# Kernel optimization log

Hardware: AMD Instinct MI355X
Metric: run time of the kernel (lower is better)

The kernel has to match this reference:

```python
import jax, jax.numpy as jnp
import numpy as np

H = 1024      # hidden_dim
NH = 16       # num_heads
HD = H // NH  # head_dim
FF = 4096     # ff_dim
EPS = 1e-6


def layer_norm(x, gamma, beta):
    # faithful to source: unbiased std (ddof=1), divide by (std + eps)
    mean = jnp.mean(x, axis=-1, keepdims=True)
    var = jnp.sum((x - mean) ** 2, axis=-1, keepdims=True) / (x.shape[-1] - 1)
    std = jnp.sqrt(var)
    return gamma * (x - mean) / (std + EPS) + beta


def linear_mulbias(x, W, b):
    # source LinearLayer: einsum('...i,io,o->...o') -> (x @ W) * b (bias MULTIPLIES)
    return jnp.einsum('bti,io->bto', x, W) * b


def setup_inputs() -> dict:
    key = jax.random.key(0)
    ks = jax.random.split(key, 11)
    B, T = 2, 2048
    return {
        'x':      jax.random.normal(ks[0], (B, T, H), jnp.float32),
        'Wqkv':   jax.random.normal(ks[1], (H, 3 * H), jnp.float32),
        'bqkv':   jax.random.normal(ks[2], (3 * H,), jnp.float32),
        'W1':     jax.random.normal(ks[3], (H, FF), jnp.float32),
        'b1':     jax.random.normal(ks[4], (FF,), jnp.float32),
        'W2':     jax.random.normal(ks[5], (FF, H), jnp.float32),
        'b2':     jax.random.normal(ks[6], (H,), jnp.float32),
        'gamma1': jax.random.normal(ks[7], (H,), jnp.float32),
        'beta1':  jax.random.normal(ks[8], (H,), jnp.float32),
        'gamma2': jax.random.normal(ks[9], (H,), jnp.float32),
        'beta2':  jax.random.normal(ks[10], (H,), jnp.float32),
    }


def attention(x, Wqkv, bqkv):
    B, T, _ = x.shape
    qkv = linear_mulbias(x, Wqkv, bqkv)                 # [B,T,3H]
    # einops 'b t (d k h) -> k b h t d' with k=3, h=NH: last dim decomposes (d,3,h)
    qkv = qkv.reshape(B, T, HD, 3, NH)
    qkv = jnp.transpose(qkv, (3, 0, 4, 1, 2))           # [3,B,NH,T,HD]
    q, k, v = qkv[0], qkv[1], qkv[2]
    scores = jnp.einsum('bhid,bhjd->bhij', q, k) / (H ** 0.5)  # scale by full hidden_dim
    attn = jax.nn.softmax(scores, axis=-1)
    out = jnp.einsum('bhij,bhjd->bhid', attn, v)        # [B,NH,T,HD]
    return jnp.transpose(out, (0, 2, 1, 3)).reshape(B, T, H)


def reference(x, Wqkv, bqkv, W1, b1, W2, b2, gamma1, beta1, gamma2, beta2):
    # dropout is identity in eval mode
    out = layer_norm(x + attention(x, Wqkv, bqkv), gamma1, beta1)
    ffn = linear_mulbias(jnp.maximum(linear_mulbias(out, W1, b1), 0.0), W2, b2)
    out = layer_norm(out + ffn, gamma2, beta2)
    return out
```

## Files before the change

### kernel.cpp

```cpp
#include <hip/hip_runtime.h>
#include <math.h>

#define B 2
#define T 2048
#define H 1024
#define NH 16
#define HD 64
#define FF 4096
#define M_TOK (B*T)
#define LOG2E 1.4426950408889634f

typedef unsigned short u16;
typedef __attribute__((ext_vector_type(8))) short bf16x8;
typedef __attribute__((ext_vector_type(4))) float f32x4;

#define WAITBAR3  asm volatile("s_waitcnt vmcnt(3)\n\ts_barrier" ::: "memory")
#define WAITBAR4  asm volatile("s_waitcnt vmcnt(4)\n\ts_barrier" ::: "memory")
#define WAITBAR0  asm volatile("s_waitcnt vmcnt(0)\n\ts_barrier" ::: "memory")

__device__ __forceinline__ u16 f2bf(float f) {
  union { float f; unsigned u; } v; v.f = f;
  const unsigned r = (v.u + 0x7FFFu + ((v.u >> 16) & 1u)) >> 16;
  return (u16)r;
}
__device__ __forceinline__ float bf2f(u16 h) {
  union { unsigned u; float f; } v; v.u = ((unsigned)h) << 16;
  return v.f;
}
__device__ __forceinline__ unsigned cvt_pk_bf16(float lo, float hi) {
  unsigned r;
  asm("v_cvt_pk_bf16_f32 %0, %1, %2" : "=v"(r) : "v"(lo), "v"(hi));
  return r;
}
__device__ __forceinline__ float m3(float a, float b, float c) {
  return fmaxf(fmaxf(a, b), c);
}
__device__ __forceinline__ void gload16(const u16* g, u16* l) {
  __builtin_amdgcn_global_load_lds(
      (const __attribute__((address_space(1))) unsigned int*)g,
      (__attribute__((address_space(3))) unsigned int*)l, 16, 0, 0);
}

__global__ __launch_bounds__(256) void preprocess(
    const float* __restrict__ x, u16* __restrict__ xh, u16* __restrict__ xl,
    const float* __restrict__ Wqkv, u16* __restrict__ WqTh, u16* __restrict__ WqTl,
    const float* __restrict__ W1_, u16* __restrict__ W1T_,
    const float* __restrict__ W2_, u16* __restrict__ W2T_)
{
  const int bid = blockIdx.x;
  const int tid = threadIdx.x;
  if (bid < 4096) {
    const size_t i = ((size_t)bid * 256 + tid) * 4;
    const float4 v = *(const float4*)(x + i);
    union { u16 s[4]; uint2 u; } h, l;
    const float f[4] = {v.x, v.y, v.z, v.w};
#pragma unroll
    for (int j = 0; j < 4; ++j) {
      const u16 hb = f2bf(f[j]); h.s[j] = hb; l.s[j] = f2bf(f[j] - bf2f(hb));
    }
    *(uint2*)(xh + i) = h.u;
    *(uint2*)(xl + i) = l.u;
    return;
  }
  __shared__ float tile[64][69];
  const float* in; u16* oh; u16* ol = nullptr; int K, N, k0, n0, split = 0;
  if (bid < 4864) {
    const int tb = bid - 4096;
    in = Wqkv; oh = WqTh; ol = WqTl; K = H; N = 3*H; split = 1;
    n0 = (tb % 48) * 64; k0 = (tb / 48) * 64;
  } else if (bid < 5888) {
    const int tb = bid - 4864;
    in = W1_; oh = W1T_; K = H; N = FF;
    n0 = (tb & 63) * 64; k0 = (tb >> 6) * 64;
  } else {
    const int tb = bid - 5888;
    in = W2_; oh = W2T_; K = FF; N = H;
    n0 = (tb & 15) * 64; k0 = (tb >> 4) * 64;
  }
  const int r = tid >> 4, c4 = (tid & 15) * 4;
#pragma unroll
  for (int i = 0; i < 4; ++i) {
    const float4 v = *(const float4*)(in + (size_t)(k0 + i*16 + r) * N + n0 + c4);
    tile[i*16+r][c4]   = v.x; tile[i*16+r][c4+1] = v.y;
    tile[i*16+r][c4+2] = v.z; tile[i*16+r][c4+3] = v.w;
  }
  __syncthreads();
  const int n = tid >> 2, kq = tid & 3;
  union { u16 s[8]; int4 v; } ph0, ph1, pl0, pl1;
#pragma unroll
  for (int j = 0; j < 8; ++j) {
    const float f0 = tile[kq*16 + j][n];
    const float f1 = tile[kq*16 + 8 + j][n];
    const u16 h0 = f2bf(f0), h1 = f2bf(f1);
    ph0.s[j] = h0; ph1.s[j] = h1;
    if (split) { pl0.s[j] = f2bf(f0 - bf2f(h0)); pl1.s[j] = f2bf(f1 - bf2f(h1)); }
  }
  u16* po = oh + (size_t)(n0 + n) * K + k0 + kq * 16;
  *(int4*)po = ph0.v; *(int4*)(po + 8) = ph1.v;
  if (split) {
    u16* pl = ol + (size_t)(n0 + n) * K + k0 + kq * 16;
    *(int4*)pl = pl0.v; *(int4*)(pl + 8) = pl1.v;
  }
}

__device__ __forceinline__ int swz(int r, int kq) {
  return r * 32 + ((kq ^ ((r >> 1) & 3)) * 8);
}

template<int SPLIT, int RELU, int OBF, int QKV3, int DEEP3, int PARTIAL>
__global__ __launch_bounds__(256) void mfma_gemm(
    const u16* __restrict__ Ah, const u16* __restrict__ Al,
    const u16* __restrict__ Bh, const u16* __restrict__ Bl,
    const float* __restrict__ bias,
    float* __restrict__ Cf, u16* __restrict__ Cb,
    int M, int N, int K)
{
  __shared__ u16 lds[DEEP3 ? 24576 : (SPLIT ? 32768 : 16384)];
  const int BUFSZ = SPLIT ? 16384 : 8192;
  const int tid = threadIdx.x;
  const int bid = blockIdx.x;
  const int xcd = bid & 7;
  const int idx = bid >> 3;
  const int row0 = (xcd * 4 + (idx & 3)) * 128;
  const int col0 = (idx >> 2) * 128;
  const int wv = tid >> 6, lane = tid & 63;
  const int wr = wv >> 1, wc = wv & 1;
  const int kq = lane >> 4, fr = lane & 15;

  int kb = 0, kE = K;
  if (PARTIAL) {
    const int khf = blockIdx.y;
    kb = khf * (K >> 1); kE = kb + (K >> 1);
    Cf += (size_t)khf * ((size_t)M * N);
  }

  f32x4 acc[4][4] = {};

#define GSTAGE(lbase, gb, rowbase, kk) do { \
    _Pragma("unroll") \
    for (int t_ = 0; t_ < 2; ++t_) { \
      const int c_ = wv * 2 + t_; \
      const int idx_ = c_ * 64 + lane; \
      const int r_ = idx_ >> 2; \
      const int kq_ = (idx_ & 3) ^ ((r_ >> 1) & 3); \
      gload16((gb) + (size_t)((rowbase) + r_) * K + (kk) + kq_ * 8, \
              &lds[(lbase) + c_ * 512]); \
    } } while (0)

#define BLSTAGE(lbase, kk) do { \
    _Pragma("unroll") \
    for (int t_ = 0; t_ < 2; ++t_) { \
      const int c_ = wv * 2 + t_; \
      if (!QKV3 || ((((col0 >> 4) + c_) % 3) != 2)) { \
        const int idx_ = c_ * 64 + lane; \
        const int r_ = idx_ >> 2; \
        const int kq_ = (idx_ & 3) ^ ((r_ >> 1) & 3); \
        gload16(Bl + (size_t)(col0 + r_) * K + (kk) + kq_ * 8, \
                &lds[(lbase) + c_ * 512]); \
      } } } while (0)

  if (DEEP3) {
    const int nk = (kE - kb) >> 5;
    GSTAGE(0, Ah, row0, kb);            GSTAGE(4096, Bh, col0, kb);
    GSTAGE(8192, Ah, row0, kb + 32);    GSTAGE(8192 + 4096, Bh, col0, kb + 32);
    WAITBAR4;
    int cslot = 0, islot = 2;
    for (int i = 0; i < nk; ++i) {
      if (i + 2 < nk) {
        const int kk = kb + (i + 2) * 32;
        GSTAGE(islot * 8192, Ah, row0, kk);
        GSTAGE(islot * 8192 + 4096, Bh, col0, kk);
        islot = (islot == 2) ? 0 : islot + 1;
      }
      const int rb = cslot * 8192;
      bf16x8 a_h[4];
#pragma unroll
      for (int m = 0; m < 4; ++m)
        a_h[m] = *(const bf16x8*)&lds[rb + swz(wr*64 + m*16 + fr, kq)];
#pragma unroll
      for (int n = 0; n < 4; ++n) {
        const bf16x8 b_h = *(const bf16x8*)&lds[rb + 4096 + swz(wc*64 + n*16 + fr, kq)];
#pragma unroll
        for (int m = 0; m < 4; ++m)
          acc[m][n] = __builtin_amdgcn_mfma_f32_16x16x32_bf16(a_h[m], b_h, acc[m][n], 0, 0, 0);
      }
      cslot = (cslot == 2) ? 0 : cslot + 1;
      if (i + 1 < nk) { if (i + 2 < nk) WAITBAR4; else WAITBAR0; }
    }
  } else {
    GSTAGE(0, Ah, row0, kb);
    GSTAGE(4096, Bh, col0, kb);
    if (SPLIT) { GSTAGE(8192, Al, row0, kb); BLSTAGE(12288, kb); }
    __syncthreads();

    int cur = 0;
    for (int k0 = kb; k0 < kE; k0 += 32) {
      const int nxt = cur ^ 1;
      if (k0 + 32 < kE) {
        GSTAGE(nxt*BUFSZ, Ah, row0, k0 + 32);
        GSTAGE(nxt*BUFSZ + 4096, Bh, col0, k0 + 32);
        if (SPLIT) { GSTAGE(nxt*BUFSZ + 8192, Al, row0, k0 + 32);
                     BLSTAGE(nxt*BUFSZ + 12288, k0 + 32); }
      }
      const int rb = cur * BUFSZ;
      bf16x8 a_h[4], a_l[4];
#pragma unroll
      for (int m = 0; m < 4; ++m) {
        a_h[m] = *(const bf16x8*)&lds[rb + swz(wr*64 + m*16 + fr, kq)];
        if (SPLIT) a_l[m] = *(const bf16x8*)&lds[rb + 8192 + swz(wr*64 + m*16 + fr, kq)];
      }
#pragma unroll
      for (int n = 0; n < 4; ++n) {
        const bf16x8 b_h = *(const bf16x8*)&lds[rb + 4096 + swz(wc*64 + n*16 + fr, kq)];
#pragma unroll
        for (int m = 0; m < 4; ++m)
          acc[m][n] = __builtin_amdgcn_mfma_f32_16x16x32_bf16(a_h[m], b_h, acc[m][n], 0, 0, 0);
        if (SPLIT) {
          const bool dolo = !QKV3 || ((((col0 >> 4) + wc * 4 + n) % 3) != 2);
          if (dolo) {
            const bf16x8 b_l = *(const bf16x8*)&lds[rb + 12288 + swz(wc*64 + n*16 + fr, kq)];
#pragma unroll
            for (int m = 0; m < 4; ++m) {
              acc[m][n] = __builtin_amdgcn_mfma_f32_16x16x32_bf16(a_h[m], b_l, acc[m][n], 0, 0, 0);
              acc[m][n] = __builtin_amdgcn_mfma_f32_16x16x32_bf16(a_l[m], b_h, acc[m][n], 0, 0, 0);
            }
          }
        }
      }
      __syncthreads();
      cur = nxt;
    }
  }
#undef GSTAGE
#undef BLSTAGE

  const int orow0 = row0 + wr * 64, ocol0 = col0 + wc * 64;
#pragma unroll
  for (int n = 0; n < 4; ++n) {
    const int col = ocol0 + n * 16 + fr;
    const float bs = PARTIAL ? 1.0f : bias[col];
#pragma unroll
    for (int m = 0; m < 4; ++m) {
      const int rbase = orow0 + m * 16 + (lane >> 4) * 4;
#pragma unroll
      for (int j = 0; j < 4; ++j) {
        float v = acc[m][n][j] * bs;
        if (RELU) v = fmaxf(v, 0.0f);
        const size_t off = (size_t)(rbase + j) * N + col;
        if (OBF) Cb[off] = f2bf(v); else Cf[off] = v;
      }
    }
  }
}

__global__ __launch_bounds__(256) void repack_qkv(
    const float* __restrict__ qkv,
    u16* __restrict__ Qh, u16* __restrict__ Ql,
    u16* __restrict__ Kh, u16* __restrict__ Kl, u16* __restrict__ Vb)
{
  const int bt = blockIdx.x;
  const int b = bt >> 11, t = bt & (T - 1);
  const int tid = threadIdx.x;
  __shared__ float Ls[3 * H];
  const float* src = qkv + (size_t)bt * (3 * H);
#pragma unroll
  for (int i = 0; i < 3; ++i) {
    const int c4 = i * 256 + tid;
    *(float4*)&Ls[c4 * 4] = *(const float4*)(src + c4 * 4);
  }
  __syncthreads();
  const float qscale = LOG2E / 32.0f;
#pragma unroll
  for (int i = 0; i < 4; ++i) {
    const int j = i * 256 + tid;
    const int h = j >> 6, d = j & 63;
    const size_t dst = (((size_t)(b * NH + h)) * T + t) * HD + d;
    const float q = Ls[d * 48 + h] * qscale;
    const u16 qhb = f2bf(q);
    Qh[dst] = qhb; Ql[dst] = f2bf(q - bf2f(qhb));
    const float k = Ls[d * 48 + 16 + h];
    const u16 khb = f2bf(k);
    Kh[dst] = khb; Kl[dst] = f2bf(k - bf2f(khb));
    Vb[dst] = f2bf(Ls[d * 48 + 32 + h]);
  }
}

__global__ __launch_bounds__(256) void vtrans(
    const u16* __restrict__ Vb, u16* __restrict__ VT)
{
  __shared__ u16 Ls[64][72];
  const int bh = blockIdx.y, t0 = blockIdx.x * 64;
  const int tid = threadIdx.x;
  const int r = tid >> 2, c = (tid & 3) * 16;
  const size_t src = ((size_t)bh * T + t0 + r) * HD + c;
  *(int4*)&Ls[r][c]     = *(const int4*)(Vb + src);
  *(int4*)&Ls[r][c + 8] = *(const int4*)(Vb + src + 8);
  __syncthreads();
  const int d = tid >> 2, tc = (tid & 3) * 16;
  u16 buf[16];
#pragma unroll
  for (int i = 0; i < 16; ++i) buf[i] = Ls[tc + i][d];
  u16* dst = VT + ((size_t)bh * HD + d) * T + t0 + tc;
  *(int4*)dst       = *(int4*)&buf[0];
  *(int4*)(dst + 8) = *(int4*)&buf[8];
}

__device__ __forceinline__ int sigma_k(int r) {
  return ((r >> 5) << 5) | (((r >> 2) & 3) << 3) | (((r >> 4) & 1) << 2) | (r & 3);
}

__global__ __launch_bounds__(512, 4) void flash_attn_mfma(
    const u16* __restrict__ Qh, const u16* __restrict__ Ql,
    const u16* __restrict__ Kh, const u16* __restrict__ Kl,
    const u16* __restrict__ VT, float* __restrict__ Out)
{
  __shared__ u16 sm[3 * 12288];
  const int i = blockIdx.x;
  const int slot = i >> 3;
  const int bh = (i & 7) * 4 + (slot >> 4);
  const int row0 = (slot & 15) * 128;
  const int b = bh >> 4, h = bh & 15;
  const int tid = threadIdx.x, wave = tid >> 6, lane = tid & 63;
  const int fr = lane & 15, kq = lane >> 4;

  bf16x8 qh[2], ql[2];
  const size_t qoff = ((size_t)bh * T + row0 + wave*16 + fr) * HD + kq*8;
#pragma unroll
  for (int ks = 0; ks < 2; ++ks) {
    qh[ks] = *(const bf16x8*)(Qh + qoff + ks*32);
    ql[ks] = *(const bf16x8*)(Ql + qoff + ks*32);
  }

  bf16x8 ones8;
#pragma unroll
  for (int z = 0; z < 8; ++z) ones8[z] = (short)0x3F80;

  f32x4 o[4] = {};
  f32x4 oex = {};
  float m_ = -1e30f;

  const int c_ = wave;
  const int r0_ = c_ * 8 + (lane >> 3), s_ = lane & 7;
  const int cd0 = s_ ^ (r0_ & 7);
  const int k0_ = sigma_k(r0_);
  const u16* pKh0 = Kh + ((size_t)bh*T + k0_)*HD + cd0*8;
  const u16* pKl0 = Kl + ((size_t)bh*T + k0_)*HD + cd0*8;
  const u16* pV0  = VT + ((size_t)bh*HD + r0_)*T + cd0*8;

#define FSTAGE(sb) do { \
    gload16(pKh0, &sm[(sb) + c_*512]); \
    gload16(pKl0, &sm[(sb) + 4096 + c_*512]); \
    gload16(pV0,  &sm[(sb) + 8192 + c_*512]); \
    pKh0 += 64*HD; pKl0 += 64*HD; pV0 += 64; \
  } while (0)

  FSTAGE(0);
  FSTAGE(12288);
  WAITBAR3;
  int cslot = 0, islot = 2;

  const int NT = T / 64;
  for (int t = 0; t < NT; ++t) {
    if (t + 2 < NT) {
      FSTAGE(islot * 12288);
      islot = (islot == 2) ? 0 : islot + 1;
    }
    const u16* smb = &sm[cslot * 12288];

    f32x4 s[4] = {};
    __builtin_amdgcn_s_setprio(1);
#pragma unroll
    for (int ks = 0; ks < 2; ++ks) {
#pragma unroll
      for (int n = 0; n < 4; ++n) {
        const int kr = n * 16 + fr;
        const int sl = ((ks*4 + kq) ^ (kr & 7)) * 8;
        const bf16x8 kh_ = *(const bf16x8*)&smb[kr*64 + sl];
        const bf16x8 kl_ = *(const bf16x8*)&smb[4096 + kr*64 + sl];
        s[n] = __builtin_amdgcn_mfma_f32_16x16x32_bf16(kh_, qh[ks], s[n], 0, 0, 0);
        s[n] = __builtin_amdgcn_mfma_f32_16x16x32_bf16(kl_, qh[ks], s[n], 0, 0, 0);
        s[n] = __builtin_amdgcn_mfma_f32_16x16x32_bf16(kh_, ql[ks], s[n], 0, 0, 0);
      }
    }
    __builtin_amdgcn_s_setprio(0);

    const float g0 = m3(s[0][0], s[0][1], s[0][2]);
    const float g1 = m3(s[0][3], s[1][0], s[1][1]);
    const float g2 = m3(s[1][2], s[1][3], s[2][0]);
    const float g3 = m3(s[2][1], s[2][2], s[2][3]);
    const float g4 = m3(s[3][0], s[3][1], s[3][2]);
    float mx = fmaxf(m3(g0, g1, g2), m3(g3, g4, s[3][3]));
    mx = fmaxf(mx, __shfl_xor(mx, 16));
    mx = fmaxf(mx, __shfl_xor(mx, 32));
    if (!__all(mx <= m_ + 8.0f)) {
      const float mn = fmaxf(m_, mx);
      const float fsc = exp2f(m_ - mn);
      m_ = mn;
#pragma unroll
      for (int n = 0; n < 4; ++n) {
        o[n][0] *= fsc; o[n][1] *= fsc;
        o[n][2] *= fsc; o[n][3] *= fsc;
      }
      oex[0] *= fsc; oex[1] *= fsc; oex[2] *= fsc; oex[3] *= fsc;
    }

    float p[4][4];
#pragma unroll
    for (int n = 0; n < 4; ++n)
#pragma unroll
      for (int jj = 0; jj < 4; ++jj)
        p[n][jj] = exp2f(s[n][jj] - m_);

    unsigned pk[4][2];
#pragma unroll
    for (int n = 0; n < 4; ++n) {
      pk[n][0] = cvt_pk_bf16(p[n][0], p[n][1]);
      pk[n][1] = cvt_pk_bf16(p[n][2], p[n][3]);
    }

    __builtin_amdgcn_s_setprio(1);
#pragma unroll
    for (int ks = 0; ks < 2; ++ks) {
      union { unsigned u[4]; bf16x8 v; } pb;
      pb.u[0] = pk[2*ks][0];   pb.u[1] = pk[2*ks][1];
      pb.u[2] = pk[2*ks+1][0]; pb.u[3] = pk[2*ks+1][1];
#pragma unroll
      for (int n = 0; n < 4; ++n) {
        const int dr = n * 16 + fr;
        const bf16x8 vf = *(const bf16x8*)&smb[8192 + dr*64 + (((ks*4 + kq) ^ (dr & 7)) * 8)];
        o[n] = __builtin_amdgcn_mfma_f32_16x16x32_bf16(vf, pb.v, o[n], 0, 0, 0);
      }
      oex = __builtin_amdgcn_mfma_f32_16x16x32_bf16(ones8, pb.v, oex, 0, 0, 0);
    }
    __builtin_amdgcn_s_setprio(0);

    cslot = (cslot == 2) ? 0 : cslot + 1;
    if (t + 1 < NT) { if (t + 2 < NT) WAITBAR3; else WAITBAR0; }
  }
#undef FSTAGE

  {
    const float inv = 1.0f / oex[0];
    const size_t qrow = (size_t)b * T + row0 + wave*16 + fr;
#pragma unroll
    for (int n = 0; n < 4; ++n) {
      float4 ov;
      ov.x = o[n][0] * inv; ov.y = o[n][1] * inv;
      ov.z = o[n][2] * inv; ov.w = o[n][3] * inv;
      *(float4*)(Out + qrow * H + h * HD + n * 16 + kq * 4) = ov;
    }
  }
}

__global__ __launch_bounds__(256) void ln_residual(
    const float* __restrict__ A, const float* __restrict__ Bz,
    const float* __restrict__ gamma, const float* __restrict__ beta,
    u16* __restrict__ obf)
{
  const int row = blockIdx.x, tid = threadIdx.x;
  const int wave = tid >> 6, lane = tid & 63;
  const size_t off = (size_t)row * H + tid * 4;
  const float4 av = *(const float4*)(A + off);
  const float4 bv = *(const float4*)(Bz + off);
  float4 y; y.x = av.x + bv.x; y.y = av.y + bv.y; y.z = av.z + bv.z; y.w = av.w + bv.w;
  float s  = y.x + y.y + y.z + y.w;
  float ss = y.x*y.x + y.y*y.y + y.z*y.z + y.w*y.w;
#pragma unroll
  for (int o = 32; o >= 1; o >>= 1) { s += __shfl_xor(s, o); ss += __shfl_xor(ss, o); }
  __shared__ float red[2][4];
  if (lane == 0) { red[0][wave] = s; red[1][wave] = ss; }
  __syncthreads();
  s  = red[0][0] + red[0][1] + red[0][2] + red[0][3];
  ss = red[1][0] + red[1][1] + red[1][2] + red[1][3];
  const float mean = s * (1.0f / (float)H);
  float var = (ss - (float)H * mean * mean) * (1.0f / (float)(H - 1));
  var = fmaxf(var, 0.0f);
  const float inv = 1.0f / (sqrtf(var) + 1e-6f);
  const float4 gv = *(const float4*)(gamma + tid * 4);
  const float4 be = *(const float4*)(beta + tid * 4);
  float4 o;
  o.x = gv.x * (y.x - mean) * inv + be.x;
  o.y = gv.y * (y.y - mean) * inv + be.y;
  o.z = gv.z * (y.z - mean) * inv + be.z;
  o.w = gv.w * (y.w - mean) * inv + be.w;
  union { u16 s[4]; uint2 u; } pk;
  pk.s[0] = f2bf(o.x); pk.s[1] = f2bf(o.y); pk.s[2] = f2bf(o.z); pk.s[3] = f2bf(o.w);
  *(uint2*)(obf + off) = pk.u;
}

__global__ __launch_bounds__(256) void ln_residual_sk(
    const u16* __restrict__ Ab, const float* __restrict__ PA,
    const float* __restrict__ PB, const float* __restrict__ bb,
    const float* __restrict__ gamma, const float* __restrict__ beta,
    float* __restrict__ out)
{
  const int row = blockIdx.x, tid = threadIdx.x;
  const int wave = tid >> 6, lane = tid & 63;
  const size_t off = (size_t)row * H + tid * 4;
  union { uint2 u; u16 s[4]; } au;
  au.u = *(const uint2*)(Ab + off);
  const float4 pa = *(const float4*)(PA + off);
  const float4 pb = *(const float4*)(PB + off);
  const float4 bw = *(const float4*)(bb + tid * 4);
  float4 y;
  y.x = bf2f(au.s[0]) + (pa.x + pb.x) * bw.x;
  y.y = bf2f(au.s[1]) + (pa.y + pb.y) * bw.y;
  y.z = bf2f(au.s[2]) + (pa.z + pb.z) * bw.z;
  y.w = bf2f(au.s[3]) + (pa.w + pb.w) * bw.w;
  float s  = y.x + y.y + y.z + y.w;
  float ss = y.x*y.x + y.y*y.y + y.z*y.z + y.w*y.w;
#pragma unroll
  for (int o = 32; o >= 1; o >>= 1) { s += __shfl_xor(s, o); ss += __shfl_xor(ss, o); }
  __shared__ float red[2][4];
  if (lane == 0) { red[0][wave] = s; red[1][wave] = ss; }
  __syncthreads();
  s  = red[0][0] + red[0][1] + red[0][2] + red[0][3];
  ss = red[1][0] + red[1][1] + red[1][2] + red[1][3];
  const float mean = s * (1.0f / (float)H);
  float var = (ss - (float)H * mean * mean) * (1.0f / (float)(H - 1));
  var = fmaxf(var, 0.0f);
  const float inv = 1.0f / (sqrtf(var) + 1e-6f);
  const float4 gv = *(const float4*)(gamma + tid * 4);
  const float4 be = *(const float4*)(beta + tid * 4);
  float4 o;
  o.x = gv.x * (y.x - mean) * inv + be.x;
  o.y = gv.y * (y.y - mean) * inv + be.y;
  o.z = gv.z * (y.z - mean) * inv + be.z;
  o.w = gv.w * (y.w - mean) * inv + be.w;
  *(float4*)(out + off) = o;
}

extern "C" void kernel_launch(void* const* d_in, const int* in_sizes, int n_in,
                              void* d_out, int out_size, void* d_ws, size_t ws_size,
                              hipStream_t stream)
{
  const float* x    = (const float*)d_in[0];
  const float* Wqkv = (const float*)d_in[1];
  const float* bqkv = (const float*)d_in[2];
  const float* W1   = (const float*)d_in[3];
  const float* b1   = (const float*)d_in[4];
  const float* W2   = (const float*)d_in[5];
  const float* b2   = (const float*)d_in[6];
  const float* g1   = (const float*)d_in[7];
  const float* be1  = (const float*)d_in[8];
  const float* g2   = (const float*)d_in[9];
  const float* be2  = (const float*)d_in[10];
  float* out = (float*)d_out;
  char* w = (char*)d_ws;

  float* qkv  = (float*)(w + 0);
  u16*   h1b  = (u16*)  (w + 0);
  u16*   xh   = (u16*)  (w + 52428800);
  u16*   xl   = (u16*)  (w + 60817408);
  u16*   Qh   = (u16*)  (w + 52428800);
  u16*   Ql   = (u16*)  (w + 60817408);
  u16*   WqTh = (u16*)  (w + 69206016);
  u16*   WqTl = (u16*)  (w + 75497472);
  u16*   Khb  = (u16*)  (w + 69206016);
  u16*   Klb  = (u16*)  (w + 77594624);
  u16*   Vbb  = (u16*)  (w + 85983232);
  u16*   VTb  = (u16*)  (w + 94371840);
  float* pAB  = (float*)(w + 52428800);
  float* attn = (float*)(w + 102760448);
  u16*   W1T  = (u16*)  (w + 119537664);
  u16*   W2T  = (u16*)  (w + 127926272);
  u16*   ln1b = (u16*)  (w + 136314880);

  preprocess<<<6912, 256, 0, stream>>>(x, xh, xl, Wqkv, WqTh, WqTl,
                                       W1, W1T, W2, W2T);
  mfma_gemm<1,0,0,1,0,0><<<24 * 32, 256, 0, stream>>>(xh, xl, WqTh, WqTl, bqkv,
                                                      qkv, nullptr, M_TOK, 3*H, H);
  repack_qkv<<<M_TOK, 256, 0, stream>>>(qkv, Qh, Ql, Khb, Klb, Vbb);
  vtrans<<<dim3(T/64, B*NH), 256, 0, stream>>>(Vbb, VTb);
  flash_attn_mfma<<<512, 512, 0, stream>>>(Qh, Ql, Khb, Klb, VTb, attn);
  ln_residual<<<M_TOK, 256, 0, stream>>>(x, attn, g1, be1, ln1b);
  mfma_gemm<0,1,1,0,1,0><<<32 * 32, 256, 0, stream>>>(ln1b, nullptr, W1T, nullptr, b1,
                                                      nullptr, h1b, M_TOK, FF, H);
  mfma_gemm<0,0,0,0,1,1><<<dim3(8 * 32, 2), 256, 0, stream>>>(h1b, nullptr, W2T, nullptr, nullptr,
                                                              pAB, nullptr, M_TOK, H, FF);
  ln_residual_sk<<<M_TOK, 256, 0, stream>>>(ln1b, pAB, pAB + 4194304, b2, g2, be2, out);
}
```

Baseline: 296.6 us.

## Fuse FFN2 split-K halves in-block via LDS and vectorize QKV repack

Replaces the two-block split-K FFN2 GEMM, which wrote two partial fp32 outputs, with a 512-thread kernel. Two wave groups each cover half of K and their accumulators are reduced through LDS, with bias and residual applied in the epilogue. The final LN then only reads one fp32 buffer instead of two partials plus the bf16 residual. Separately, repack_qkv pads its LDS row to avoid bank conflicts and writes 4-element packed stores instead of scalar u16 stores. The costs are larger LDS per block and fewer blocks in flight for FFN2 (256 blocks of 512 threads).

Measured after the change: 292.2 us. No clear change (-1.5%).

```diff
diff --git a/kernel.cpp b/kernel.cpp
--- a/kernel.cpp
+++ b/kernel.cpp
@@ -107,7 +107,7 @@
   return r * 32 + ((kq ^ ((r >> 1) & 3)) * 8);
 }
 
-template<int SPLIT, int RELU, int OBF, int QKV3, int DEEP3, int PARTIAL>
+template<int SPLIT, int RELU, int OBF, int QKV3, int DEEP3>
 __global__ __launch_bounds__(256) void mfma_gemm(
     const u16* __restrict__ Ah, const u16* __restrict__ Al,
     const u16* __restrict__ Bh, const u16* __restrict__ Bl,
@@ -127,13 +127,6 @@
   const int wr = wv >> 1, wc = wv & 1;
   const int kq = lane >> 4, fr = lane & 15;
 
-  int kb = 0, kE = K;
-  if (PARTIAL) {
-    const int khf = blockIdx.y;
-    kb = khf * (K >> 1); kE = kb + (K >> 1);
-    Cf += (size_t)khf * ((size_t)M * N);
-  }
-
   f32x4 acc[4][4] = {};
 
 #define GSTAGE(lbase, gb, rowbase, kk) do { \
@@ -160,14 +153,14 @@
       } } } while (0)
 
   if (DEEP3) {
-    const int nk = (kE - kb) >> 5;
-    GSTAGE(0, Ah, row0, kb);            GSTAGE(4096, Bh, col0, kb);
-    GSTAGE(8192, Ah, row0, kb + 32);    GSTAGE(8192 + 4096, Bh, col0, kb + 32);
+    const int nk = K >> 5;
+    GSTAGE(0, Ah, row0, 0);            GSTAGE(4096, Bh, col0, 0);
+    GSTAGE(8192, Ah, row0, 32);        GSTAGE(8192 + 4096, Bh, col0, 32);
     WAITBAR4;
     int cslot = 0, islot = 2;
     for (int i = 0; i < nk; ++i) {
       if (i + 2 < nk) {
-        const int kk = kb + (i + 2) * 32;
+        const int kk = (i + 2) * 32;
         GSTAGE(islot * 8192, Ah, row0, kk);
         GSTAGE(islot * 8192 + 4096, Bh, col0, kk);
         islot = (islot == 2) ? 0 : islot + 1;
@@ -188,15 +181,15 @@
       if (i + 1 < nk) { if (i + 2 < nk) WAITBAR4; else WAITBAR0; }
     }
   } else {
-    GSTAGE(0, Ah, row0, kb);
-    GSTAGE(4096, Bh, col0, kb);
-    if (SPLIT) { GSTAGE(8192, Al, row0, kb); BLSTAGE(12288, kb); }
+    GSTAGE(0, Ah, row0, 0);
+    GSTAGE(4096, Bh, col0, 0);
+    if (SPLIT) { GSTAGE(8192, Al, row0, 0); BLSTAGE(12288, 0); }
     __syncthreads();
 
     int cur = 0;
-    for (int k0 = kb; k0 < kE; k0 += 32) {
+    for (int k0 = 0; k0 < K; k0 += 32) {
       const int nxt = cur ^ 1;
-      if (k0 + 32 < kE) {
+      if (k0 + 32 < K) {
         GSTAGE(nxt*BUFSZ, Ah, row0, k0 + 32);
         GSTAGE(nxt*BUFSZ + 4096, Bh, col0, k0 + 32);
         if (SPLIT) { GSTAGE(nxt*BUFSZ + 8192, Al, row0, k0 + 32);
@@ -238,7 +231,7 @@
 #pragma unroll
   for (int n = 0; n < 4; ++n) {
     const int col = ocol0 + n * 16 + fr;
-    const float bs = PARTIAL ? 1.0f : bias[col];
+    const float bs = bias[col];
 #pragma unroll
     for (int m = 0; m < 4; ++m) {
       const int rbase = orow0 + m * 16 + (lane >> 4) * 4;
@@ -253,6 +246,101 @@
   }
 }
 
+__global__ __launch_bounds__(512, 2) void mfma_ffn2(
+    const u16* __restrict__ Ah, const u16* __restrict__ Bh,
+    const u16* __restrict__ Res, const float* __restrict__ bias,
+    float* __restrict__ Y)
+{
+  const int N = H, K = FF;
+  __shared__ u16 lds[2 * 24576];
+  const int tid = threadIdx.x;
+  const int bid = blockIdx.x;
+  const int xcd = bid & 7;
+  const int idx = bid >> 3;
+  const int row0 = (xcd * 4 + (idx & 3)) * 128;
+  const int col0 = (idx >> 2) * 128;
+  const int wv8 = tid >> 6, lane = tid & 63;
+  const int grp = wv8 >> 2, wv = wv8 & 3;
+  const int wr = wv >> 1, wc = wv & 1;
+  const int kq = lane >> 4, fr = lane & 15;
+  const int kb = grp * (K >> 1);
+  u16* gl = &lds[grp * 24576];
+
+  f32x4 acc[4][4] = {};
+
+#define GSTAGE2(lbase, gb, rowbase, kk) do { \
+    _Pragma("unroll") \
+    for (int t_ = 0; t_ < 2; ++t_) { \
+      const int c_ = wv * 2 + t_; \
+      const int idx_ = c_ * 64 + lane; \
+      const int r_ = idx_ >> 2; \
+      const int kq_ = (idx_ & 3) ^ ((r_ >> 1) & 3); \
+      gload16((gb) + (size_t)((rowbase) + r_) * K + (kk) + kq_ * 8, \
+              &gl[(lbase) + c_ * 512]); \
+    } } while (0)
+
+  const int nk = (K >> 1) >> 5;
+  GSTAGE2(0, Ah, row0, kb);            GSTAGE2(4096, Bh, col0, kb);
+  GSTAGE2(8192, Ah, row0, kb + 32);    GSTAGE2(8192 + 4096, Bh, col0, kb + 32);
+  WAITBAR4;
+  int cslot = 0, islot = 2;
+  for (int i = 0; i < nk; ++i) {
+    if (i + 2 < nk) {
+      const int kk = kb + (i + 2) * 32;
+      GSTAGE2(islot * 8192, Ah, row0, kk);
+      GSTAGE2(islot * 8192 + 4096, Bh, col0, kk);
+      islot = (islot == 2) ? 0 : islot + 1;
+    }
+    const int rb = cslot * 8192;
+    bf16x8 a_h[4];
+#pragma unroll
+    for (int m = 0; m < 4; ++m)
+      a_h[m] = *(const bf16x8*)&gl[rb + swz(wr*64 + m*16 + fr, kq)];
+#pragma unroll
+    for (int n = 0; n < 4; ++n) {
+      const bf16x8 b_h = *(const bf16x8*)&gl[rb + 4096 + swz(wc*64 + n*16 + fr, kq)];
+#pragma unroll
+      for (int m = 0; m < 4; ++m)
+        acc[m][n] = __builtin_amdgcn_mfma_f32_16x16x32_bf16(a_h[m], b_h, acc[m][n], 0, 0, 0);
+    }
+    cslot = (cslot == 2) ? 0 : cslot + 1;
+    if (i + 1 < nk) { if (i + 2 < nk) WAITBAR4; else WAITBAR0; }
+  }
+#undef GSTAGE2
+
+  __syncthreads();
+  float* fm = (float*)lds;
+  const int base = wv * 4096;
+  if (grp == 1) {
+#pragma unroll
+    for (int m = 0; m < 4; ++m)
+#pragma unroll
+      for (int n = 0; n < 4; ++n)
+        *(f32x4*)&fm[base + (m*4 + n)*256 + lane*4] = acc[m][n];
+  }
+  __syncthreads();
+  if (grp == 0) {
+    const int orow0 = row0 + wr * 64, ocol0 = col0 + wc * 64;
+#pragma unroll
+    for (int n = 0; n < 4; ++n) {
+      const int col = ocol0 + n * 16 + fr;
+      const float bs = bias[col];
+#pragma unroll
+      for (int m = 0; m < 4; ++m) {
+        const f32x4 ob = *(const f32x4*)&fm[base + (m*4 + n)*256 + lane*4];
+        const int rbase = orow0 + m * 16 + kq * 4;
+#pragma unroll
+        for (int j = 0; j < 4; ++j) {
+          const size_t off = (size_t)(rbase + j) * N + col;
+          Y[off] = bf2f(Res[off]) + (acc[m][n][j] + ob[j]) * bs;
+        }
+      }
+    }
+  }
+}
+
+__device__ __forceinline__ int padi(int o) { return o + 4 * (o >> 6); }
+
 __global__ __launch_bounds__(256) void repack_qkv(
     const float* __restrict__ qkv,
     u16* __restrict__ Qh, u16* __restrict__ Ql,
@@ -261,28 +349,35 @@
   const int bt = blockIdx.x;
   const int b = bt >> 11, t = bt & (T - 1);
   const int tid = threadIdx.x;
-  __shared__ float Ls[3 * H];
+  __shared__ float Ls[3 * H + 192];
   const float* src = qkv + (size_t)bt * (3 * H);
 #pragma unroll
   for (int i = 0; i < 3; ++i) {
-    const int c4 = i * 256 + tid;
-    *(float4*)&Ls[c4 * 4] = *(const float4*)(src + c4 * 4);
+    const int o = (i * 256 + tid) * 4;
+    *(float4*)&Ls[padi(o)] = *(const float4*)(src + o);
   }
   __syncthreads();
   const float qscale = LOG2E / 32.0f;
-#pragma unroll
-  for (int i = 0; i < 4; ++i) {
-    const int j = i * 256 + tid;
-    const int h = j >> 6, d = j & 63;
-    const size_t dst = (((size_t)(b * NH + h)) * T + t) * HD + d;
-    const float q = Ls[d * 48 + h] * qscale;
+  const int h = tid >> 4, d0 = (tid & 15) * 4;
+  const size_t dst = (((size_t)(b * NH + h)) * T + t) * HD + d0;
+  union { u16 s[4]; uint2 u; } qh_, ql_, kh_, kl_, vb_;
+#pragma unroll
+  for (int jj = 0; jj < 4; ++jj) {
+    const int ob = (d0 + jj) * 48 + h;
+    const float q = Ls[padi(ob)] * qscale;
+    const float k = Ls[padi(ob + 16)];
+    const float v = Ls[padi(ob + 32)];
     const u16 qhb = f2bf(q);
-    Qh[dst] = qhb; Ql[dst] = f2bf(q - bf2f(qhb));
-    const float k = Ls[d * 48 + 16 + h];
+    qh_.s[jj] = qhb; ql_.s[jj] = f2bf(q - bf2f(qhb));
     const u16 khb = f2bf(k);
-    Kh[dst] = khb; Kl[dst] = f2bf(k - bf2f(khb));
-    Vb[dst] = f2bf(Ls[d * 48 + 32 + h]);
-  }
+    kh_.s[jj] = khb; kl_.s[jj] = f2bf(k - bf2f(khb));
+    vb_.s[jj] = f2bf(v);
+  }
+  *(uint2*)(Qh + dst) = qh_.u;
+  *(uint2*)(Ql + dst) = ql_.u;
+  *(uint2*)(Kh + dst) = kh_.u;
+  *(uint2*)(Kl + dst) = kl_.u;
+  *(uint2*)(Vb + dst) = vb_.u;
 }
 
 __global__ __launch_bounds__(256) void vtrans(
@@ -488,25 +583,15 @@
   *(uint2*)(obf + off) = pk.u;
 }
 
-__global__ __launch_bounds__(256) void ln_residual_sk(
-    const u16* __restrict__ Ab, const float* __restrict__ PA,
-    const float* __restrict__ PB, const float* __restrict__ bb,
+__global__ __launch_bounds__(256) void ln_only(
+    const float* __restrict__ Yv,
     const float* __restrict__ gamma, const float* __restrict__ beta,
     float* __restrict__ out)
 {
   const int row = blockIdx.x, tid = threadIdx.x;
   const int wave = tid >> 6, lane = tid & 63;
   const size_t off = (size_t)row * H + tid * 4;
-  union { uint2 u; u16 s[4]; } au;
-  au.u = *(const uint2*)(Ab + off);
-  const float4 pa = *(const float4*)(PA + off);
-  const float4 pb = *(const float4*)(PB + off);
-  const float4 bw = *(const float4*)(bb + tid * 4);
-  float4 y;
-  y.x = bf2f(au.s[0]) + (pa.x + pb.x) * bw.x;
-  y.y = bf2f(au.s[1]) + (pa.y + pb.y) * bw.y;
-  y.z = bf2f(au.s[2]) + (pa.z + pb.z) * bw.z;
-  y.w = bf2f(au.s[3]) + (pa.w + pb.w) * bw.w;
+  const float4 y = *(const float4*)(Yv + off);
   float s  = y.x + y.y + y.z + y.w;
   float ss = y.x*y.x + y.y*y.y + y.z*y.z + y.w*y.w;
 #pragma unroll
@@ -560,23 +645,22 @@
   u16*   Klb  = (u16*)  (w + 77594624);
   u16*   Vbb  = (u16*)  (w + 85983232);
   u16*   VTb  = (u16*)  (w + 94371840);
-  float* pAB  = (float*)(w + 52428800);
   float* attn = (float*)(w + 102760448);
+  float* Yb   = (float*)(w + 102760448);
   u16*   W1T  = (u16*)  (w + 119537664);
   u16*   W2T  = (u16*)  (w + 127926272);
   u16*   ln1b = (u16*)  (w + 136314880);
 
   preprocess<<<6912, 256, 0, stream>>>(x, xh, xl, Wqkv, WqTh, WqTl,
                                        W1, W1T, W2, W2T);
-  mfma_gemm<1,0,0,1,0,0><<<24 * 32, 256, 0, stream>>>(xh, xl, WqTh, WqTl, bqkv,
-                                                      qkv, nullptr, M_TOK, 3*H, H);
+  mfma_gemm<1,0,0,1,0><<<24 * 32, 256, 0, stream>>>(xh, xl, WqTh, WqTl, bqkv,
+                                                    qkv, nullptr, M_TOK, 3*H, H);
   repack_qkv<<<M_TOK, 256, 0, stream>>>(qkv, Qh, Ql, Khb, Klb, Vbb);
   vtrans<<<dim3(T/64, B*NH), 256, 0, stream>>>(Vbb, VTb);
   flash_attn_mfma<<<512, 512, 0, stream>>>(Qh, Ql, Khb, Klb, VTb, attn);
   ln_residual<<<M_TOK, 256, 0, stream>>>(x, attn, g1, be1, ln1b);
-  mfma_gemm<0,1,1,0,1,0><<<32 * 32, 256, 0, stream>>>(ln1b, nullptr, W1T, nullptr, b1,
-                                                      nullptr, h1b, M_TOK, FF, H);
-  mfma_gemm<0,0,0,0,1,1><<<dim3(8 * 32, 2), 256, 0, stream>>>(h1b, nullptr, W2T, nullptr, nullptr,
-                                                              pAB, nullptr, M_TOK, H, FF);
-  ln_residual_sk<<<M_TOK, 256, 0, stream>>>(ln1b, pAB, pAB + 4194304, b2, g2, be2, out);
-}
+  mfma_gemm<0,1,1,0,1><<<32 * 32, 256, 0, stream>>>(ln1b, nullptr, W1T, nullptr, b1,
+                                                    nullptr, h1b, M_TOK, FF, H);
+  mfma_ffn2<<<256, 512, 0, stream>>>(h1b, W2T, ln1b, b2, Yb);
+  ln_only<<<M_TOK, 256, 0, stream>>>(Yb, g2, be2, out);
+}
```
